# Kernel tuning notes

Measured on AMD Instinct MI355X. Metric: run time of the kernel, lower is better.

## Reference

```python
import jax, jax.numpy as jnp
import numpy as np

B, S, H = 128, 1024, 256
NEG = 1e9

def setup_inputs() -> dict:
    key = jax.random.key(0)
    ks = jax.random.split(key, 11)
    sc = 0.05
    return {
        'ref': jax.random.normal(ks[0], (B, S, H), jnp.float32),
        'query': jax.random.normal(ks[1], (B, H), jnp.float32),
        'mask': jax.random.randint(ks[2], (B, S), 0, 2, jnp.int32),
        'wg': jax.random.normal(ks[3], (H, H), jnp.float32) * sc,
        'bg': jax.random.normal(ks[4], (H,), jnp.float32) * sc,
        'wqg': jax.random.normal(ks[5], (H, H), jnp.float32) * sc,
        'vg': jax.random.normal(ks[6], (H,), jnp.float32) * sc,
        'wp': jax.random.normal(ks[7], (H, H), jnp.float32) * sc,
        'bp': jax.random.normal(ks[8], (H,), jnp.float32) * sc,
        'wqp': jax.random.normal(ks[9], (H, H), jnp.float32) * sc,
        'vp': jax.random.normal(ks[10], (H,), jnp.float32) * sc,
    }

def reference(ref, query, mask, wg, bg, wqg, vg, wp, bp, wqp, vp):
    # Bahdanau additive pointer attention with glimpse, per PointerDecoder.pointer_net
    maskf = mask.astype(ref.dtype)
    # glimpse attention
    enc_g = jnp.einsum('bsd,hd->bsh', ref, wg) + bg            # conv1d kernel=1
    q_g = jnp.einsum('bd,hd->bh', query, wqg)                   # w_q_g (no bias)
    scores_g = jnp.einsum('bsh,h->bs', jnp.tanh(enc_g + q_g[:, None, :]), vg)
    att_g = jax.nn.softmax(scores_g - maskf * NEG, axis=-1)     # [B,S]
    glimpse = jnp.einsum('bs,bsd->bd', att_g, ref) + query      # [B,H]
    # pointer scores
    enc_p = jnp.einsum('bsd,hd->bsh', ref, wp) + bp
    q_p = jnp.einsum('bd,hd->bh', glimpse, wqp)
    scores_p = jnp.einsum('bsh,h->bs', jnp.tanh(enc_p + q_p[:, None, :]), vp)
    masked_scores = scores_p - maskf * NEG                      # [B,S]
    return masked_scores
```

## Files before the change

kernel.cpp:

```cpp
#include <hip/hip_runtime.h>

#define Bb 128
#define Ss 1024
#define Hh 256
#define NEGF 1e9f

typedef short bf16x8 __attribute__((ext_vector_type(8)));
typedef float f32x4 __attribute__((ext_vector_type(4)));

__device__ __forceinline__ short f2bf(float f) {
    union { float f; unsigned u; } c; c.f = f;
    return (short)((c.u + 0x8000u) >> 16);
}

__device__ __forceinline__ unsigned cvt_pk_bf16(float a, float b) {
    unsigned r;
    asm("v_cvt_pk_bf16_f32 %0, %1, %2" : "=v"(r) : "v"(a), "v"(b));
    return r;
}

__device__ __forceinline__ float fast_tanh(float x) {
    float cl = fminf(fmaxf(x, -10.f), 10.f);
    float e = __expf(2.f * cl);
    return (e - 1.f) * __builtin_amdgcn_rcpf(e + 1.f);
}

__device__ __forceinline__ void stage16(const void* g, short* l) {
    __builtin_amdgcn_global_load_lds((const __attribute__((address_space(1))) void*)g,
                                     (__attribute__((address_space(3))) void*)l, 16, 0, 0);
}

#define WAITVM(N) { __builtin_amdgcn_s_waitcnt(0x0F70 | (N)); __builtin_amdgcn_sched_barrier(0); }

__global__ __launch_bounds__(256) void prep_kernel(const float* __restrict__ wg,
                                                   const float* __restrict__ wp,
                                                   const float* __restrict__ query,
                                                   const float* __restrict__ wqg,
                                                   const float* __restrict__ bg,
                                                   short* __restrict__ wgb,
                                                   short* __restrict__ wpb,
                                                   float* __restrict__ qbias_g) {
    int blk = blockIdx.x, t = threadIdx.x;
    if (blk < 256) {
        int i = blk * 256 + t;
        wgb[i] = f2bf(wg[i]);
        wpb[i] = f2bf(wp[i]);
    } else {
        int b = blk - 256;
        const float4* qr = (const float4*)(query + b * Hh);
        const float4* wr = (const float4*)(wqg + t * Hh);
        float acc = 0.f;
#pragma unroll 8
        for (int i = 0; i < Hh / 4; ++i) {
            float4 q4 = qr[i], w4 = wr[i];
            acc += q4.x * w4.x + q4.y * w4.y + q4.z * w4.z + q4.w * w4.w;
        }
        qbias_g[b * Hh + t] = acc + bg[t];
    }
}

template <int MASKED, int LOADF32>
__global__ __launch_bounds__(512, 2) void scores_mfma(const float* __restrict__ reff,
                                                      const short* __restrict__ refb_in,
                                                      const short* __restrict__ Wbf,
                                                      const float* __restrict__ qbias,
                                                      const float* __restrict__ vvec,
                                                      const int* __restrict__ mask,
                                                      float* __restrict__ out) {
    constexpr int TS = LOADF32 ? 8192 : 4096;
    constexpr int I = LOADF32 ? 2 : 1;
    __shared__ __align__(16) short Abuf[4][TS];
    __shared__ float partial[8][256];
    const int t = threadIdx.x;
    const int w = t >> 6;
    const int lane = t & 63;
    const int nl = lane & 15;
    const int quad = lane >> 4;
    const int b = blockIdx.x >> 2;
    const int row0 = (blockIdx.x & 3) * 256;

    bf16x8 bfrag[2][8];
#pragma unroll
    for (int nc2 = 0; nc2 < 2; ++nc2) {
        const short* wpr = Wbf + (w * 32 + nc2 * 16 + nl) * Hh + quad * 8;
#pragma unroll
        for (int kb = 0; kb < 8; ++kb)
            bfrag[nc2][kb] = *(const bf16x8*)(wpr + kb * 32);
    }
    const float qb0 = qbias[b * Hh + w * 32 + nl];
    const float qb1 = qbias[b * Hh + w * 32 + 16 + nl];
    const float vv0 = vvec[w * 32 + nl];
    const float vv1 = vvec[w * 32 + 16 + nl];

    auto stage_tile = [&](int tt, int buf) {
        if (LOADF32) {
            const float* g = reff + ((size_t)b * Ss + row0 + tt * 16 + nl) * Hh + w * 32 + quad * 8;
            stage16(g,     &Abuf[buf][(w * 2 + 0) * 512]);
            stage16(g + 4, &Abuf[buf][(w * 2 + 1) * 512]);
        } else {
            const short* g = refb_in + ((size_t)b * Ss + row0 + tt * 16 + nl) * Hh + w * 32 + quad * 8;
            stage16(g, &Abuf[buf][w * 512]);
        }
    };

    stage_tile(0, 0);
    stage_tile(1, 1);
    stage_tile(2, 2);

#pragma unroll 1
    for (int tt = 0; tt < 16; ++tt) {
        if (tt <= 13)      WAITVM(2 * I)
        else if (tt == 14) WAITVM(I)
        else               WAITVM(0)
        __builtin_amdgcn_s_barrier();
        __builtin_amdgcn_sched_barrier(0);
        if (tt <= 12) stage_tile(tt + 3, (tt + 3) & 3);

        const short* bufp = Abuf[tt & 3];
        f32x4 c0 = {0.f, 0.f, 0.f, 0.f};
        f32x4 c1 = {0.f, 0.f, 0.f, 0.f};
#pragma unroll
        for (int kb = 0; kb < 8; ++kb) {
            bf16x8 af;
            if (LOADF32) {
                float4 lo = *(const float4*)&bufp[(kb * 2 + 0) * 512 + lane * 8];
                float4 hi = *(const float4*)&bufp[(kb * 2 + 1) * 512 + lane * 8];
                union { unsigned u[4]; bf16x8 v; } cv;
                cv.u[0] = cvt_pk_bf16(lo.x, lo.y);
                cv.u[1] = cvt_pk_bf16(lo.z, lo.w);
                cv.u[2] = cvt_pk_bf16(hi.x, hi.y);
                cv.u[3] = cvt_pk_bf16(hi.z, hi.w);
                af = cv.v;
            } else {
                af = *(const bf16x8*)&bufp[kb * 512 + lane * 8];
            }
            c0 = __builtin_amdgcn_mfma_f32_16x16x32_bf16(af, bfrag[0][kb], c0, 0, 0, 0);
            c1 = __builtin_amdgcn_mfma_f32_16x16x32_bf16(af, bfrag[1][kb], c1, 0, 0, 0);
        }
#pragma unroll
        for (int r = 0; r < 4; ++r) {
            float s = fast_tanh(c0[r] + qb0) * vv0 + fast_tanh(c1[r] + qb1) * vv1;
            s += __shfl_xor(s, 1, 64);
            s += __shfl_xor(s, 2, 64);
            s += __shfl_xor(s, 4, 64);
            s += __shfl_xor(s, 8, 64);
            if (nl == 0) partial[w][tt * 16 + quad * 4 + r] = s;
        }
    }

    __syncthreads();
    if (t < 256) {
        float s = 0.f;
#pragma unroll
        for (int g = 0; g < 8; ++g) s += partial[g][t];
        if (MASKED) s -= (float)mask[b * Ss + row0 + t] * NEGF;
        out[(size_t)b * Ss + row0 + t] = s;
    }
}

__global__ __launch_bounds__(1024) void softmax_kernel(const float* __restrict__ scores,
                                                       const int* __restrict__ mask,
                                                       float* __restrict__ att) {
    int b = blockIdx.x, t = threadIdx.x;
    __shared__ float red[16];
    int idx = b * Ss + t;
    float x = scores[idx] - (float)mask[idx] * NEGF;

    float m = x;
#pragma unroll
    for (int o = 1; o < 64; o <<= 1) m = fmaxf(m, __shfl_xor(m, o, 64));
    if ((t & 63) == 0) red[t >> 6] = m;
    __syncthreads();
    float M = red[0];
#pragma unroll
    for (int j = 1; j < 16; ++j) M = fmaxf(M, red[j]);
    __syncthreads();

    float e = __expf(x - M);
    float s = e;
#pragma unroll
    for (int o = 1; o < 64; o <<= 1) s += __shfl_xor(s, o, 64);
    if ((t & 63) == 0) red[t >> 6] = s;
    __syncthreads();
    float S = 0.f;
#pragma unroll
    for (int j = 0; j < 16; ++j) S += red[j];

    att[idx] = e * __builtin_amdgcn_rcpf(S);
}

__global__ __launch_bounds__(256) void glimpse_part(const float* __restrict__ reff,
                                                    const float* __restrict__ att,
                                                    short* __restrict__ refb_out,
                                                    float* __restrict__ gpart) {
    int b = blockIdx.x, q = blockIdx.y, t = threadIdx.x;
    const int c = t & 31;
    const int rg = t >> 5;
    __shared__ float part[8][Hh];
    const float* base = reff + ((size_t)(b * Ss + q * 128)) * Hh;
    short* outb = refb_out + ((size_t)(b * Ss + q * 128)) * Hh;
    const float* ap = att + b * Ss + q * 128;

    float acc[8] = {0.f, 0.f, 0.f, 0.f, 0.f, 0.f, 0.f, 0.f};
#pragma unroll 4
    for (int it = 0; it < 16; ++it) {
        int row = it * 8 + rg;
        float a = ap[row];
        const float4* rp = (const float4*)(base + (size_t)row * Hh + c * 8);
        float4 lo = rp[0], hi = rp[1];
        acc[0] += a * lo.x; acc[1] += a * lo.y; acc[2] += a * lo.z; acc[3] += a * lo.w;
        acc[4] += a * hi.x; acc[5] += a * hi.y; acc[6] += a * hi.z; acc[7] += a * hi.w;
        union { unsigned u[4]; bf16x8 v; } cv;
        cv.u[0] = cvt_pk_bf16(lo.x, lo.y);
        cv.u[1] = cvt_pk_bf16(lo.z, lo.w);
        cv.u[2] = cvt_pk_bf16(hi.x, hi.y);
        cv.u[3] = cvt_pk_bf16(hi.z, hi.w);
        *(bf16x8*)(outb + (size_t)row * Hh + c * 8) = cv.v;
    }
#pragma unroll
    for (int j = 0; j < 8; ++j) part[rg][c * 8 + j] = acc[j];
    __syncthreads();
    float s = 0.f;
#pragma unroll
    for (int g = 0; g < 8; ++g) s += part[g][t];
    gpart[(size_t)(b * 8 + q) * Hh + t] = s;
}

__global__ __launch_bounds__(256) void qbias_p_kernel(const float* __restrict__ gpart,
                                                      const float* __restrict__ query,
                                                      const float* __restrict__ wqp,
                                                      const float* __restrict__ bp,
                                                      float* __restrict__ out) {
    int b = blockIdx.x, t = threadIdx.x;
    __shared__ __align__(16) float gl[Hh];
    float g = query[b * Hh + t];
#pragma unroll
    for (int q = 0; q < 8; ++q) g += gpart[(b * 8 + q) * Hh + t];
    gl[t] = g;
    __syncthreads();
    const float4* wr = (const float4*)(wqp + t * Hh);
    const float4* gp = (const float4*)gl;
    float acc = 0.f;
#pragma unroll 8
    for (int i = 0; i < Hh / 4; ++i) {
        float4 w4 = wr[i];
        float4 g4 = gp[i];
        acc += w4.x * g4.x + w4.y * g4.y + w4.z * g4.z + w4.w * g4.w;
    }
    out[b * Hh + t] = acc + bp[t];
}

extern "C" void kernel_launch(void* const* d_in, const int* in_sizes, int n_in,
                              void* d_out, int out_size, void* d_ws, size_t ws_size,
                              hipStream_t stream) {
    const float* ref   = (const float*)d_in[0];
    const float* query = (const float*)d_in[1];
    const int*   mask  = (const int*)d_in[2];
    const float* wg    = (const float*)d_in[3];
    const float* bg    = (const float*)d_in[4];
    const float* wqg   = (const float*)d_in[5];
    const float* vg    = (const float*)d_in[6];
    const float* wp    = (const float*)d_in[7];
    const float* bp    = (const float*)d_in[8];
    const float* wqp   = (const float*)d_in[9];
    const float* vp    = (const float*)d_in[10];
    float* out = (float*)d_out;

    char* ws = (char*)d_ws;
    short* ref_bf   = (short*)(ws + 0);
    size_t off = (size_t)Bb * Ss * Hh * 2;
    short* wg_bf    = (short*)(ws + off);               off += 131072;
    short* wp_bf    = (short*)(ws + off);               off += 131072;
    float* qbias_g  = (float*)(ws + off);               off += 131072;
    float* qbias_p  = (float*)(ws + off);               off += 131072;
    float* scores_g = (float*)(ws + off);               off += 524288;
    float* att      = (float*)(ws + off);               off += 524288;
    float* gpart    = (float*)(ws + off);

    prep_kernel<<<384, 256, 0, stream>>>(wg, wp, query, wqg, bg, wg_bf, wp_bf, qbias_g);
    scores_mfma<0, 1><<<512, 512, 0, stream>>>(
        ref, nullptr, wg_bf, qbias_g, vg, nullptr, scores_g);
    softmax_kernel<<<Bb, Ss, 0, stream>>>(scores_g, mask, att);
    glimpse_part<<<dim3(Bb, 8), 256, 0, stream>>>(ref, att, ref_bf, gpart);
    qbias_p_kernel<<<Bb, Hh, 0, stream>>>(gpart, query, wqp, bp, qbias_p);
    scores_mfma<1, 0><<<512, 512, 0, stream>>>(
        nullptr, ref_bf, wp_bf, qbias_p, vp, mask, out);
}
```

Before: 304.3 us.

## Drop bf16 ref copy; convert fp32 tiles to bf16 in LDS once per tile

The glimpse kernel no longer writes a bf16 copy of ref, and the pointer-score pass reads fp32 ref directly instead. The MFMA kernel now stages fp32 tiles in a double buffer and converts each tile to bf16 once into a triple-buffered LDS area, rather than converting inside the MFMA inner loop. This removes the bf16 write pass and the redundant per-warp conversions. In exchange, the second scoring pass reads twice as many bytes and each tile adds an extra LDS write and synchronization step.

Result: no change. 303.6 us (-0.2%).

```diff
diff --git a/kernel.cpp b/kernel.cpp
--- a/kernel.cpp
+++ b/kernel.cpp
@@ -59,17 +59,15 @@
     }
 }
 
-template <int MASKED, int LOADF32>
+template <int MASKED>
 __global__ __launch_bounds__(512, 2) void scores_mfma(const float* __restrict__ reff,
-                                                      const short* __restrict__ refb_in,
                                                       const short* __restrict__ Wbf,
                                                       const float* __restrict__ qbias,
                                                       const float* __restrict__ vvec,
                                                       const int* __restrict__ mask,
                                                       float* __restrict__ out) {
-    constexpr int TS = LOADF32 ? 8192 : 4096;
-    constexpr int I = LOADF32 ? 2 : 1;
-    __shared__ __align__(16) short Abuf[4][TS];
+    __shared__ __align__(16) short F32buf[2][8192];
+    __shared__ __align__(16) short Bbuf[3][4096];
     __shared__ float partial[8][256];
     const int t = threadIdx.x;
     const int w = t >> 6;
@@ -92,48 +90,47 @@
     const float vv0 = vvec[w * 32 + nl];
     const float vv1 = vvec[w * 32 + 16 + nl];
 
-    auto stage_tile = [&](int tt, int buf) {
-        if (LOADF32) {
-            const float* g = reff + ((size_t)b * Ss + row0 + tt * 16 + nl) * Hh + w * 32 + quad * 8;
-            stage16(g,     &Abuf[buf][(w * 2 + 0) * 512]);
-            stage16(g + 4, &Abuf[buf][(w * 2 + 1) * 512]);
-        } else {
-            const short* g = refb_in + ((size_t)b * Ss + row0 + tt * 16 + nl) * Hh + w * 32 + quad * 8;
-            stage16(g, &Abuf[buf][w * 512]);
-        }
+    auto stage = [&](int tt, int f) {
+        const float* g = reff + ((size_t)b * Ss + row0 + tt * 16 + nl) * Hh + w * 32 + quad * 8;
+        stage16(g,     &F32buf[f][(w * 2 + 0) * 512]);
+        stage16(g + 4, &F32buf[f][(w * 2 + 1) * 512]);
     };
-
-    stage_tile(0, 0);
-    stage_tile(1, 1);
-    stage_tile(2, 2);
+    auto convert = [&](int f, int bb) {
+        float4 lo = *(const float4*)&F32buf[f][(w * 2 + 0) * 512 + lane * 8];
+        float4 hi = *(const float4*)&F32buf[f][(w * 2 + 1) * 512 + lane * 8];
+        union { unsigned u[4]; bf16x8 v; } cv;
+        cv.u[0] = cvt_pk_bf16(lo.x, lo.y);
+        cv.u[1] = cvt_pk_bf16(lo.z, lo.w);
+        cv.u[2] = cvt_pk_bf16(hi.x, hi.y);
+        cv.u[3] = cvt_pk_bf16(hi.z, hi.w);
+        *(bf16x8*)&Bbuf[bb][w * 512 + lane * 8] = cv.v;
+    };
+
+    stage(0, 0);
+    stage(1, 1);
+    WAITVM(2)
+    convert(0, 0);
+    asm volatile("s_waitcnt lgkmcnt(0)" ::: "memory");
+    __builtin_amdgcn_s_barrier();
+    __builtin_amdgcn_sched_barrier(0);
 
 #pragma unroll 1
     for (int tt = 0; tt < 16; ++tt) {
-        if (tt <= 13)      WAITVM(2 * I)
-        else if (tt == 14) WAITVM(I)
-        else               WAITVM(0)
+        if (tt <= 13) stage(tt + 2, tt & 1);
+        if (tt <= 14) {
+            if (tt <= 13) WAITVM(2) else WAITVM(0)
+            convert((tt + 1) & 1, (tt + 1) % 3);
+        }
+        asm volatile("s_waitcnt lgkmcnt(0)" ::: "memory");
         __builtin_amdgcn_s_barrier();
         __builtin_amdgcn_sched_barrier(0);
-        if (tt <= 12) stage_tile(tt + 3, (tt + 3) & 3);
-
-        const short* bufp = Abuf[tt & 3];
+
+        const short* bufp = Bbuf[tt % 3];
         f32x4 c0 = {0.f, 0.f, 0.f, 0.f};
         f32x4 c1 = {0.f, 0.f, 0.f, 0.f};
 #pragma unroll
         for (int kb = 0; kb < 8; ++kb) {
-            bf16x8 af;
-            if (LOADF32) {
-                float4 lo = *(const float4*)&bufp[(kb * 2 + 0) * 512 + lane * 8];
-                float4 hi = *(const float4*)&bufp[(kb * 2 + 1) * 512 + lane * 8];
-                union { unsigned u[4]; bf16x8 v; } cv;
-                cv.u[0] = cvt_pk_bf16(lo.x, lo.y);
-                cv.u[1] = cvt_pk_bf16(lo.z, lo.w);
-                cv.u[2] = cvt_pk_bf16(hi.x, hi.y);
-                cv.u[3] = cvt_pk_bf16(hi.z, hi.w);
-                af = cv.v;
-            } else {
-                af = *(const bf16x8*)&bufp[kb * 512 + lane * 8];
-            }
+            bf16x8 af = *(const bf16x8*)&bufp[kb * 512 + lane * 8];
             c0 = __builtin_amdgcn_mfma_f32_16x16x32_bf16(af, bfrag[0][kb], c0, 0, 0, 0);
             c1 = __builtin_amdgcn_mfma_f32_16x16x32_bf16(af, bfrag[1][kb], c1, 0, 0, 0);
         }
@@ -191,14 +188,12 @@
 
 __global__ __launch_bounds__(256) void glimpse_part(const float* __restrict__ reff,
                                                     const float* __restrict__ att,
-                                                    short* __restrict__ refb_out,
                                                     float* __restrict__ gpart) {
     int b = blockIdx.x, q = blockIdx.y, t = threadIdx.x;
     const int c = t & 31;
     const int rg = t >> 5;
     __shared__ float part[8][Hh];
     const float* base = reff + ((size_t)(b * Ss + q * 128)) * Hh;
-    short* outb = refb_out + ((size_t)(b * Ss + q * 128)) * Hh;
     const float* ap = att + b * Ss + q * 128;
 
     float acc[8] = {0.f, 0.f, 0.f, 0.f, 0.f, 0.f, 0.f, 0.f};
@@ -210,12 +205,6 @@
         float4 lo = rp[0], hi = rp[1];
         acc[0] += a * lo.x; acc[1] += a * lo.y; acc[2] += a * lo.z; acc[3] += a * lo.w;
         acc[4] += a * hi.x; acc[5] += a * hi.y; acc[6] += a * hi.z; acc[7] += a * hi.w;
-        union { unsigned u[4]; bf16x8 v; } cv;
-        cv.u[0] = cvt_pk_bf16(lo.x, lo.y);
-        cv.u[1] = cvt_pk_bf16(lo.z, lo.w);
-        cv.u[2] = cvt_pk_bf16(hi.x, hi.y);
-        cv.u[3] = cvt_pk_bf16(hi.z, hi.w);
-        *(bf16x8*)(outb + (size_t)row * Hh + c * 8) = cv.v;
     }
 #pragma unroll
     for (int j = 0; j < 8; ++j) part[rg][c * 8 + j] = acc[j];
@@ -267,8 +256,7 @@
     float* out = (float*)d_out;
 
     char* ws = (char*)d_ws;
-    short* ref_bf   = (short*)(ws + 0);
-    size_t off = (size_t)Bb * Ss * Hh * 2;
+    size_t off = 0;
     short* wg_bf    = (short*)(ws + off);               off += 131072;
     short* wp_bf    = (short*)(ws + off);               off += 131072;
     float* qbias_g  = (float*)(ws + off);               off += 131072;
@@ -278,11 +266,9 @@
     float* gpart    = (float*)(ws + off);
 
     prep_kernel<<<384, 256, 0, stream>>>(wg, wp, query, wqg, bg, wg_bf, wp_bf, qbias_g);
-    scores_mfma<0, 1><<<512, 512, 0, stream>>>(
-        ref, nullptr, wg_bf, qbias_g, vg, nullptr, scores_g);
+    scores_mfma<0><<<512, 512, 0, stream>>>(ref, wg_bf, qbias_g, vg, nullptr, scores_g);
     softmax_kernel<<<Bb, Ss, 0, stream>>>(scores_g, mask, att);
-    glimpse_part<<<dim3(Bb, 8), 256, 0, stream>>>(ref, att, ref_bf, gpart);
+    glimpse_part<<<dim3(Bb, 8), 256, 0, stream>>>(ref, att, gpart);
     qbias_p_kernel<<<Bb, Hh, 0, stream>>>(gpart, query, wqp, bp, qbias_p);
-    scores_mfma<1, 0><<<512, 512, 0, stream>>>(
-        nullptr, ref_bf, wp_bf, qbias_p, vp, mask, out);
-}
+    scores_mfma<1><<<512, 512, 0, stream>>>(ref, wp_bf, qbias_p, vp, mask, out);
+}
```
